# Kernel optimization log

Hardware: AMD Instinct MI355X
Metric: run time of the kernel (lower is better)

## Reference

```python
import jax, jax.numpy as jnp
import numpy as np

B, T, C, H = 2, 2048, 1024, 16
HS = C // H        # head dim = 64
HALF = HS // 2     # rope half = 32


def _rope_cos_sin():
    # standard RoPE frequencies over the half-dim
    inv_freq = 1.0 / (10000.0 ** (np.arange(HALF, dtype=np.float32) / HALF))
    t = np.arange(T, dtype=np.float32)
    ang = np.outer(t, inv_freq)  # [T, HALF]
    cos = np.cos(ang)[None, None]  # [1,1,T,HALF]
    sin = np.sin(ang)[None, None]
    return jnp.asarray(cos), jnp.asarray(sin)


def setup_inputs() -> dict:
    key = jax.random.key(0)
    k1, k2, k3 = jax.random.split(key, 3)
    cos, sin = _rope_cos_sin()
    return {
        "x": jax.random.normal(k1, (B, T, C), dtype=jnp.float32),
        "cos": cos,
        "sin": sin,
        "w_attn": jax.random.normal(k2, (C, 3 * C), dtype=jnp.float32) * (1.0 / np.sqrt(C)),
        "b_attn": jnp.zeros((3 * C,), dtype=jnp.float32),
        "w_proj": jax.random.normal(k3, (C, C), dtype=jnp.float32) * (1.0 / np.sqrt(C)),
        "b_proj": jnp.zeros((C,), dtype=jnp.float32),
    }


def _rope_apply(x, cos, sin):
    # x: [B,H,T,HS]; cos/sin: [1,1,T,HALF]
    x1, x2 = x[..., :HALF], x[..., HALF:]
    return jnp.concatenate([x1 * cos - x2 * sin, x1 * sin + x2 * cos], axis=-1)


def reference(x, cos, sin, w_attn, b_attn, w_proj, b_proj):
    b, t, c = x.shape
    qkv = x @ w_attn + b_attn                      # [B,T,3C]
    q, k, v = jnp.split(qkv, 3, axis=-1)
    # [B,T,C] -> [B,H,T,HS]
    def to_heads(u):
        return u.reshape(b, t, H, HS).transpose(0, 2, 1, 3)
    q, k, v = to_heads(q), to_heads(k), to_heads(v)
    q = _rope_apply(q, cos[:, :, :t], sin[:, :, :t])
    k = _rope_apply(k, cos[:, :, :t], sin[:, :, :t])
    scale = 1.0 / np.sqrt(HS).astype(np.float32)
    scores = jnp.einsum("bhqd,bhkd->bhqk", q, k) * scale
    causal = jnp.tril(jnp.ones((t, t), dtype=bool))
    scores = jnp.where(causal, scores, jnp.finfo(scores.dtype).min)
    attn = jax.nn.softmax(scores, axis=-1)
    ctx = jnp.einsum("bhqk,bhkd->bhqd", attn, v)   # [B,H,T,HS]
    ctx = ctx.transpose(0, 2, 1, 3).reshape(b, t, c)
    return ctx @ w_proj + b_proj
```

## Files before the change

kernel.cpp:

```cpp
#include <hip/hip_runtime.h>
#include <hip/hip_bf16.h>

#define Bn    2
#define Tdim  2048
#define Cdim  1024
#define Hn    16
#define HSd   64
#define Mrows 4096

typedef unsigned short u16;
typedef __attribute__((ext_vector_type(8))) short short8;
typedef __attribute__((ext_vector_type(4))) float f32x4;

__device__ __forceinline__ u16 f2bf(float f) {
  union { __hip_bfloat16 h; u16 u; } cv;
  cv.h = __float2bfloat16(f);
  return cv.u;
}

#define GLOAD_LDS16(g, l)                                                     \
  __builtin_amdgcn_global_load_lds(                                           \
      (const __attribute__((address_space(1))) void*)(g),                     \
      (__attribute__((address_space(3))) void*)(l), 16, 0, 0)

__global__ __launch_bounds__(256) void k_convert_x(const float* __restrict__ x,
                                                   u16* __restrict__ xb) {
  int i = blockIdx.x * 256 + threadIdx.x;
  float4 v = ((const float4*)x)[i];
  unsigned o0 = (unsigned)f2bf(v.x) | ((unsigned)f2bf(v.y) << 16);
  unsigned o1 = (unsigned)f2bf(v.z) | ((unsigned)f2bf(v.w) << 16);
  ((uint2*)xb)[i] = make_uint2(o0, o1);
}

__global__ __launch_bounds__(256) void k_transpose_w(const float* __restrict__ in,
                                                     u16* __restrict__ out,
                                                     int R, int Cc) {
  __shared__ float tile[64][65];
  int c0 = blockIdx.x * 64, r0 = blockIdx.y * 64;
  int lc = threadIdx.x & 63, l0 = threadIdx.x >> 6;
  for (int rr = l0; rr < 64; rr += 4)
    tile[rr][lc] = in[(size_t)(r0 + rr) * Cc + c0 + lc];
  __syncthreads();
  for (int rr = l0; rr < 64; rr += 4)
    out[(size_t)(c0 + rr) * R + r0 + lc] = f2bf(tile[lc][rr]);
}

__global__ __launch_bounds__(256) void k_transpose_v(const u16* __restrict__ Vh,
                                                     u16* __restrict__ Vt) {
  __shared__ u16 tile[64][72];
  int bh = blockIdx.y, t0 = blockIdx.x * 64;
  int lc = threadIdx.x & 63, l0 = threadIdx.x >> 6;
  const u16* src = Vh + (size_t)bh * Tdim * HSd;
  u16* dst = Vt + (size_t)bh * HSd * Tdim;
  for (int rr = l0; rr < 64; rr += 4)
    tile[rr][lc] = src[(size_t)(t0 + rr) * HSd + lc];
  __syncthreads();
  for (int dd = l0; dd < 64; dd += 4)
    dst[(size_t)dd * Tdim + t0 + lc] = tile[lc][dd];
}

template <int EPI>
__global__ __launch_bounds__(256, 2) void k_gemm(
    const u16* __restrict__ A, const u16* __restrict__ Bt,
    const float* __restrict__ bias, const float* __restrict__ cosT,
    const float* __restrict__ sinT, u16* __restrict__ Qh, u16* __restrict__ Kh,
    u16* __restrict__ Vh, float* __restrict__ Out, int Ndim, int Kdim) {
  __shared__ u16 As[128 * 32];
  __shared__ u16 Bs[128 * 32];
  const int tid = threadIdx.x;
  const int wid = tid >> 6, lane = tid & 63;
  const int m0 = blockIdx.x * 128, n0 = blockIdx.y * 128;
  const int wm = (wid >> 1) * 64, wn = (wid & 1) * 64;
  const int lr = lane & 15, lg = lane >> 4;

  f32x4 acc[4][4] = {};

  const u16* Ag = A + (size_t)m0 * Kdim;
  const u16* Bg = Bt + (size_t)n0 * Kdim;
  const int srow = lane >> 2, ske = (lane & 3) * 8;

  for (int k0 = 0; k0 < Kdim; k0 += 32) {
    for (int c = wid; c < 8; c += 4) {
      int row = c * 16 + srow;
      GLOAD_LDS16(Ag + (size_t)row * Kdim + k0 + ske, As + c * 512);
      GLOAD_LDS16(Bg + (size_t)row * Kdim + k0 + ske, Bs + c * 512);
    }
    __syncthreads();
    short8 a[4], b[4];
#pragma unroll
    for (int i = 0; i < 4; i++)
      a[i] = *(const short8*)(As + (wm + i * 16 + lr) * 32 + 8 * lg);
#pragma unroll
    for (int j = 0; j < 4; j++)
      b[j] = *(const short8*)(Bs + (wn + j * 16 + lr) * 32 + 8 * lg);
#pragma unroll
    for (int i = 0; i < 4; i++)
#pragma unroll
      for (int j = 0; j < 4; j++)
        acc[i][j] =
            __builtin_amdgcn_mfma_f32_16x16x32_bf16(a[i], b[j], acc[i][j], 0, 0, 0);
    __syncthreads();
  }

  const int nbase = n0 + wn;
  if (EPI == 0) {
    const int sec = nbase >> 10;
    const int hh = (nbase & 1023) >> 6;
    const float qs = (sec == 0) ? 0.125f : 1.0f;
    float bj[4];
#pragma unroll
    for (int j = 0; j < 4; j++) bj[j] = bias[nbase + j * 16 + lr];
#pragma unroll
    for (int i = 0; i < 4; i++) {
      int growb = m0 + wm + i * 16 + 4 * lg;
#pragma unroll
      for (int r = 0; r < 4; r++) {
        int gr = growb + r;
        int bI = gr >> 11, t = gr & (Tdim - 1);
        size_t off = ((size_t)(bI * Hn + hh) * Tdim + t) * HSd;
        if (sec < 2) {
          u16* dst = (sec == 0) ? Qh : Kh;
#pragma unroll
          for (int j = 0; j < 2; j++) {
            int d = j * 16 + lr;
            float v1 = acc[i][j][r] + bj[j];
            float v2 = acc[i][j + 2][r] + bj[j + 2];
            float cs = cosT[t * 32 + d], sn = sinT[t * 32 + d];
            dst[off + d] = f2bf((v1 * cs - v2 * sn) * qs);
            dst[off + d + 32] = f2bf((v1 * sn + v2 * cs) * qs);
          }
        } else {
#pragma unroll
          for (int j = 0; j < 4; j++)
            Vh[off + j * 16 + lr] = f2bf(acc[i][j][r] + bj[j]);
        }
      }
    }
  } else {
#pragma unroll
    for (int i = 0; i < 4; i++) {
      int growb = m0 + wm + i * 16 + 4 * lg;
#pragma unroll
      for (int r = 0; r < 4; r++) {
        int gr = growb + r;
#pragma unroll
        for (int j = 0; j < 4; j++) {
          int col = nbase + j * 16 + lr;
          Out[(size_t)gr * Ndim + col] = acc[i][j][r] + bias[col];
        }
      }
    }
  }
}

__global__ __launch_bounds__(512, 4) void k_attn(const u16* __restrict__ Qh,
                                                 const u16* __restrict__ Kh,
                                                 const u16* __restrict__ Vt,
                                                 u16* __restrict__ ctx) {
  __shared__ u16 Ks[2][64 * 64];
  __shared__ u16 Vs[2][64 * 64];
  __shared__ u16 Plds[8][16][72];
  const int tid = threadIdx.x;
  const int wid = tid >> 6, lane = tid & 63;
  const int lr = lane & 15, lg = lane >> 4;
  const int bid = blockIdx.x;
  const int xb = 15 - (bid >> 5);
  const int bh = bid & 31;
  const int qr0 = xb * 128 + wid * 16;
  const int nt = 2 * xb + 2;
  const int itd = qr0 >> 6;
  const u16* Q = Qh + (size_t)bh * Tdim * HSd;
  const u16* K = Kh + (size_t)bh * Tdim * HSd;
  const u16* V = Vt + (size_t)bh * HSd * Tdim;

  short8 qf0 = *(const short8*)(Q + (size_t)(qr0 + lr) * HSd + 8 * lg);
  short8 qf1 = *(const short8*)(Q + (size_t)(qr0 + lr) * HSd + 32 + 8 * lg);

  const int srow = lane >> 3;
  const int scol = 16 * ((lane & 7) ^ srow);
  const int swz = (lr & 7) << 4;

  f32x4 ctxa[4] = {};
  float m2[4] = {-1e30f, -1e30f, -1e30f, -1e30f};
  float m2L[4] = {-1e30f, -1e30f, -1e30f, -1e30f};
  float ssum[4] = {0.f, 0.f, 0.f, 0.f};
  const float L2E = 1.44269504089f;
  const f32x4 zero = {};

#define STAGE_KV(b, kv0)                                                      \
  do {                                                                        \
    GLOAD_LDS16((const char*)(K + (size_t)((kv0) + wid * 8 + srow) * HSd) +   \
                    scol,                                                     \
                Ks[b] + wid * 8 * 64);                                        \
    GLOAD_LDS16((const char*)(V + (size_t)(wid * 8 + srow) * Tdim + (kv0)) +  \
                    scol,                                                     \
                Vs[b] + wid * 8 * 64);                                        \
  } while (0)

  STAGE_KV(0, 0);
  __syncthreads();

  int cur = 0;
  for (int it = 0; it < nt; ++it) {
    const int kv0 = it * 64;
    if (it + 1 < nt) STAGE_KV(cur ^ 1, kv0 + 64);

    if (it <= itd) {
      const char* ksb = (const char*)(Ks[cur]);
      const char* vsb = (const char*)(Vs[cur]);

      f32x4 s[4];
#pragma unroll
      for (int f = 0; f < 4; ++f) {
        int row = 16 * f + lr;
        int c0 = (lg * 16) ^ swz;
        short8 kf0 = *(const short8*)(ksb + row * 128 + c0);
        short8 kf1 = *(const short8*)(ksb + row * 128 + (c0 ^ 64));
        s[f] = __builtin_amdgcn_mfma_f32_16x16x32_bf16(qf0, kf0, zero, 0, 0, 0);
        s[f] = __builtin_amdgcn_mfma_f32_16x16x32_bf16(qf1, kf1, s[f], 0, 0, 0);
      }

      float sv[4][4], tm[4];
#pragma unroll
      for (int r = 0; r < 4; ++r) {
        if (it == itd) {
          int q = qr0 + 4 * lg + r;
#pragma unroll
          for (int f = 0; f < 4; ++f)
            sv[f][r] = (kv0 + 16 * f + lr <= q) ? s[f][r] : -1e30f;
        } else {
#pragma unroll
          for (int f = 0; f < 4; ++f) sv[f][r] = s[f][r];
        }
        float t = fmaxf(fmaxf(sv[0][r], sv[1][r]), fmaxf(sv[2][r], sv[3][r]));
        t = fmaxf(t, __shfl_xor(t, 1));
        t = fmaxf(t, __shfl_xor(t, 2));
        t = fmaxf(t, __shfl_xor(t, 4));
        t = fmaxf(t, __shfl_xor(t, 8));
        tm[r] = t;
      }

      bool up = (tm[0] > m2[0]) | (tm[1] > m2[1]) | (tm[2] > m2[2]) |
                (tm[3] > m2[3]);
      if (__any(up)) {
#pragma unroll
        for (int r = 0; r < 4; ++r) {
          float mn = fmaxf(m2[r], tm[r]);
          float alpha = __builtin_amdgcn_exp2f((m2[r] - mn) * L2E);
          m2[r] = mn;
          m2L[r] = mn * L2E;
          ssum[r] *= alpha;
#pragma unroll
          for (int dt = 0; dt < 4; ++dt) ctxa[dt][r] *= alpha;
        }
      }

#pragma unroll
      for (int r = 0; r < 4; ++r) {
#pragma unroll
        for (int f = 0; f < 4; ++f) {
          float p = __builtin_amdgcn_exp2f(fmaf(sv[f][r], L2E, -m2L[r]));
          ssum[r] += p;
          Plds[wid][4 * lg + r][16 * f + lr] = f2bf(p);
        }
      }

      const char* pb = (const char*)(&Plds[wid][0][0]);
      short8 pa0 = *(const short8*)(pb + lr * 144 + lg * 16);
      short8 pa1 = *(const short8*)(pb + lr * 144 + 64 + lg * 16);

#pragma unroll
      for (int dt = 0; dt < 4; ++dt) {
        int row = 16 * dt + lr;
        int c0 = (lg * 16) ^ swz;
        short8 vb0 = *(const short8*)(vsb + row * 128 + c0);
        short8 vb1 = *(const short8*)(vsb + row * 128 + (c0 ^ 64));
        ctxa[dt] =
            __builtin_amdgcn_mfma_f32_16x16x32_bf16(pa0, vb0, ctxa[dt], 0, 0, 0);
        ctxa[dt] =
            __builtin_amdgcn_mfma_f32_16x16x32_bf16(pa1, vb1, ctxa[dt], 0, 0, 0);
      }
    }

    __syncthreads();
    cur ^= 1;
  }
#undef STAGE_KV

  const int bI = bh >> 4, hh = bh & 15;
#pragma unroll
  for (int r = 0; r < 4; ++r) {
    float s = ssum[r];
    s += __shfl_xor(s, 1);
    s += __shfl_xor(s, 2);
    s += __shfl_xor(s, 4);
    s += __shfl_xor(s, 8);
    float inv = 1.0f / s;
    int t = qr0 + 4 * lg + r;
    size_t off = ((size_t)bI * Tdim + t) * Cdim + hh * HSd;
#pragma unroll
    for (int dt = 0; dt < 4; dt++)
      ctx[off + dt * 16 + lr] = f2bf(ctxa[dt][r] * inv);
  }
}

extern "C" void kernel_launch(void* const* d_in, const int* in_sizes, int n_in,
                              void* d_out, int out_size, void* d_ws,
                              size_t ws_size, hipStream_t stream) {
  const float* x = (const float*)d_in[0];
  const float* cosT = (const float*)d_in[1];
  const float* sinT = (const float*)d_in[2];
  const float* wattn = (const float*)d_in[3];
  const float* battn = (const float*)d_in[4];
  const float* wproj = (const float*)d_in[5];
  const float* bproj = (const float*)d_in[6];
  float* out = (float*)d_out;
  char* ws = (char*)d_ws;
  const size_t MB = 1024 * 1024;
  u16* xb = (u16*)(ws + 0);
  u16* Vt = (u16*)(ws + 0);
  u16* wattnT = (u16*)(ws + 8 * MB);
  u16* wprojT = (u16*)(ws + 14 * MB);
  u16* Qh = (u16*)(ws + 16 * MB);
  u16* Kh = (u16*)(ws + 24 * MB);
  u16* Vh = (u16*)(ws + 32 * MB);
  u16* ctx = (u16*)(ws + 40 * MB);

  k_convert_x<<<4096, 256, 0, stream>>>(x, xb);
  k_transpose_w<<<dim3(48, 16), 256, 0, stream>>>(wattn, wattnT, 1024, 3072);
  k_transpose_w<<<dim3(16, 16), 256, 0, stream>>>(wproj, wprojT, 1024, 1024);
  k_gemm<0><<<dim3(32, 24), 256, 0, stream>>>(xb, wattnT, battn, cosT, sinT, Qh,
                                              Kh, Vh, nullptr, 3072, 1024);
  k_transpose_v<<<dim3(32, 32), 256, 0, stream>>>(Vh, Vt);
  k_attn<<<512, 512, 0, stream>>>(Qh, Kh, Vt, ctx);
  k_gemm<1><<<dim3(32, 8), 256, 0, stream>>>(ctx, wprojT, bproj, nullptr,
                                             nullptr, nullptr, nullptr, nullptr,
                                             out, 1024, 1024);
}
```

Baseline: 225.5 us.

## Double-buffer GEMM LDS tiles with K=64 steps and XOR swizzle

The bf16 GEMM kernel now stages 64-wide K tiles into two LDS buffers and prefetches the next tile with direct global-to-LDS loads while computing on the current one. This removes one of the two barriers per iteration and halves the loop trip count. An XOR swizzle on the 16-byte column chunks is meant to cut LDS bank conflicts on the fragment reads. LDS use grows from 16KB to 64KB per block, which can limit how many blocks fit per CU under the launch bound of two.

```diff
diff --git a/kernel.cpp b/kernel.cpp
--- a/kernel.cpp
+++ b/kernel.cpp
@@ -65,42 +65,69 @@
     const float* __restrict__ bias, const float* __restrict__ cosT,
     const float* __restrict__ sinT, u16* __restrict__ Qh, u16* __restrict__ Kh,
     u16* __restrict__ Vh, float* __restrict__ Out, int Ndim, int Kdim) {
-  __shared__ u16 As[128 * 32];
-  __shared__ u16 Bs[128 * 32];
+  __shared__ u16 As[2][128 * 64];
+  __shared__ u16 Bs[2][128 * 64];
   const int tid = threadIdx.x;
   const int wid = tid >> 6, lane = tid & 63;
   const int m0 = blockIdx.x * 128, n0 = blockIdx.y * 128;
   const int wm = (wid >> 1) * 64, wn = (wid & 1) * 64;
   const int lr = lane & 15, lg = lane >> 4;
+  const int swz = (lr & 7) << 4;
 
   f32x4 acc[4][4] = {};
 
   const u16* Ag = A + (size_t)m0 * Kdim;
   const u16* Bg = Bt + (size_t)n0 * Kdim;
-  const int srow = lane >> 2, ske = (lane & 3) * 8;
-
-  for (int k0 = 0; k0 < Kdim; k0 += 32) {
-    for (int c = wid; c < 8; c += 4) {
-      int row = c * 16 + srow;
-      GLOAD_LDS16(Ag + (size_t)row * Kdim + k0 + ske, As + c * 512);
-      GLOAD_LDS16(Bg + (size_t)row * Kdim + k0 + ske, Bs + c * 512);
-    }
+  const int sr8 = lane >> 3;
+  const int scol = 16 * ((lane & 7) ^ sr8);
+
+#define STAGE_G(b, k0)                                                        \
+  do {                                                                        \
+    _Pragma("unroll") for (int c = 0; c < 4; ++c) {                           \
+      int row = c * 32 + wid * 8 + sr8;                                       \
+      GLOAD_LDS16((const char*)(Ag + (size_t)row * Kdim + (k0)) + scol,       \
+                  (u16*)As[b] + (c * 32 + wid * 8) * 64);                     \
+      GLOAD_LDS16((const char*)(Bg + (size_t)row * Kdim + (k0)) + scol,       \
+                  (u16*)Bs[b] + (c * 32 + wid * 8) * 64);                     \
+    }                                                                         \
+  } while (0)
+
+  const int nt = Kdim >> 6;
+  STAGE_G(0, 0);
+  __syncthreads();
+  int cur = 0;
+  for (int t = 0; t < nt; ++t) {
+    if (t + 1 < nt) STAGE_G(cur ^ 1, (t + 1) * 64);
+    const char* ab = (const char*)As[cur];
+    const char* bb = (const char*)Bs[cur];
+    short8 a[4][2], b[4][2];
+#pragma unroll
+    for (int i = 0; i < 4; i++) {
+      int ra = (wm + i * 16 + lr) * 128;
+#pragma unroll
+      for (int kk = 0; kk < 2; kk++)
+        a[i][kk] = *(const short8*)(ab + ra + ((kk * 64 + lg * 16) ^ swz));
+    }
+#pragma unroll
+    for (int j = 0; j < 4; j++) {
+      int rb = (wn + j * 16 + lr) * 128;
+#pragma unroll
+      for (int kk = 0; kk < 2; kk++)
+        b[j][kk] = *(const short8*)(bb + rb + ((kk * 64 + lg * 16) ^ swz));
+    }
+#pragma unroll
+    for (int i = 0; i < 4; i++)
+#pragma unroll
+      for (int j = 0; j < 4; j++) {
+        acc[i][j] = __builtin_amdgcn_mfma_f32_16x16x32_bf16(a[i][0], b[j][0],
+                                                            acc[i][j], 0, 0, 0);
+        acc[i][j] = __builtin_amdgcn_mfma_f32_16x16x32_bf16(a[i][1], b[j][1],
+                                                            acc[i][j], 0, 0, 0);
+      }
     __syncthreads();
-    short8 a[4], b[4];
-#pragma unroll
-    for (int i = 0; i < 4; i++)
-      a[i] = *(const short8*)(As + (wm + i * 16 + lr) * 32 + 8 * lg);
-#pragma unroll
-    for (int j = 0; j < 4; j++)
-      b[j] = *(const short8*)(Bs + (wn + j * 16 + lr) * 32 + 8 * lg);
-#pragma unroll
-    for (int i = 0; i < 4; i++)
-#pragma unroll
-      for (int j = 0; j < 4; j++)
-        acc[i][j] =
-            __builtin_amdgcn_mfma_f32_16x16x32_bf16(a[i], b[j], acc[i][j], 0, 0, 0);
-    __syncthreads();
+    cur ^= 1;
   }
+#undef STAGE_G
 
   const int nbase = n0 + wn;
   if (EPI == 0) {
```

New measurement: 229.9 us. Within noise of the previous version (+2.0%).

## Rewrite GEMM with 256x256 tiles, 4-stage async LDS pipeline and swizzle

Applied to the files above, without the earlier changes.

Replaces the 128x128 single-buffered GEMM with a 512-thread 256x256 tile kernel that prefetches three K-steps ahead into a 4-deep LDS ring using direct global-to-LDS loads. It adds an XOR swizzle against LDS bank conflicts and splits each K-step into two MFMA phases with explicit barriers, waitcnts and priority hints. The aim is to hide global load latency and raise data reuse per block. In exchange, both launches use far fewer blocks (192 and 64), which may underfill the GPU.

```diff
diff --git a/kernel.cpp b/kernel.cpp
--- a/kernel.cpp
+++ b/kernel.cpp
@@ -22,6 +22,8 @@
   __builtin_amdgcn_global_load_lds(                                           \
       (const __attribute__((address_space(1))) void*)(g),                     \
       (__attribute__((address_space(3))) void*)(l), 16, 0, 0)
+
+#define CFENCE asm volatile("" ::: "memory")
 
 __global__ __launch_bounds__(256) void k_convert_x(const float* __restrict__ x,
                                                    u16* __restrict__ xb) {
@@ -60,93 +62,157 @@
 }
 
 template <int EPI>
-__global__ __launch_bounds__(256, 2) void k_gemm(
+__global__ __launch_bounds__(512, 2) void k_gemm(
     const u16* __restrict__ A, const u16* __restrict__ Bt,
     const float* __restrict__ bias, const float* __restrict__ cosT,
     const float* __restrict__ sinT, u16* __restrict__ Qh, u16* __restrict__ Kh,
     u16* __restrict__ Vh, float* __restrict__ Out, int Ndim, int Kdim) {
-  __shared__ u16 As[128 * 32];
-  __shared__ u16 Bs[128 * 32];
+  __shared__ u16 As[4][8192];
+  __shared__ u16 Bs[4][8192];
   const int tid = threadIdx.x;
   const int wid = tid >> 6, lane = tid & 63;
-  const int m0 = blockIdx.x * 128, n0 = blockIdx.y * 128;
-  const int wm = (wid >> 1) * 64, wn = (wid & 1) * 64;
+  const int wr = wid >> 2, wc = wid & 3;
   const int lr = lane & 15, lg = lane >> 4;
-
-  f32x4 acc[4][4] = {};
+  const int m0 = blockIdx.x * 256, n0 = blockIdx.y * 256;
+
+  f32x4 acc[8][4] = {};
 
   const u16* Ag = A + (size_t)m0 * Kdim;
   const u16* Bg = Bt + (size_t)n0 * Kdim;
-  const int srow = lane >> 2, ske = (lane & 3) * 8;
-
-  for (int k0 = 0; k0 < Kdim; k0 += 32) {
-    for (int c = wid; c < 8; c += 4) {
-      int row = c * 16 + srow;
-      GLOAD_LDS16(Ag + (size_t)row * Kdim + k0 + ske, As + c * 512);
-      GLOAD_LDS16(Bg + (size_t)row * Kdim + k0 + ske, Bs + c * 512);
+  const int sgr = wid * 16 + (lane >> 2);
+  const int scb = ((lane & 3) ^ ((lane >> 3) & 3)) << 4;
+
+#define STAGE_A(b, t, i)                                                      \
+  GLOAD_LDS16((const char*)(Ag + (size_t)((i)*128 + sgr) * Kdim + (t)*32) +   \
+                  scb,                                                        \
+              As[b] + (i)*4096 + wid * 512)
+#define STAGE_B(b, t, i)                                                      \
+  GLOAD_LDS16((const char*)(Bg + (size_t)((i)*128 + sgr) * Kdim + (t)*32) +   \
+                  scb,                                                        \
+              Bs[b] + (i)*4096 + wid * 512)
+
+#define LDFRAG(buf, row)                                                      \
+  (*(const short8*)((const char*)(buf) + (row)*64 +                           \
+                    ((lg * 16) ^ ((((row) >> 1) & 3) << 4))))
+
+  const int nt = Kdim >> 5;
+#pragma unroll
+  for (int t = 0; t < 3; ++t) {
+    STAGE_A(t, t, 0);
+    STAGE_A(t, t, 1);
+    STAGE_B(t, t, 0);
+    STAGE_B(t, t, 1);
+  }
+  asm volatile("s_waitcnt vmcnt(8)" ::: "memory");
+  __builtin_amdgcn_s_barrier();
+  CFENCE;
+
+  for (int t = 0; t < nt; ++t) {
+    const u16* ab = As[t & 3];
+    const u16* bb = Bs[t & 3];
+    const int bst = (t + 3) & 3;
+    const bool do_stage = (t + 3 < nt);
+    short8 a[4], b[4];
+#pragma unroll
+    for (int mi = 0; mi < 4; ++mi) a[mi] = LDFRAG(ab, wr * 128 + mi * 16 + lr);
+#pragma unroll
+    for (int nj = 0; nj < 4; ++nj) b[nj] = LDFRAG(bb, wc * 64 + nj * 16 + lr);
+    if (do_stage) {
+      STAGE_A(bst, t + 3, 0);
+      STAGE_A(bst, t + 3, 1);
     }
-    __syncthreads();
-    short8 a[4], b[4];
-#pragma unroll
-    for (int i = 0; i < 4; i++)
-      a[i] = *(const short8*)(As + (wm + i * 16 + lr) * 32 + 8 * lg);
-#pragma unroll
-    for (int j = 0; j < 4; j++)
-      b[j] = *(const short8*)(Bs + (wn + j * 16 + lr) * 32 + 8 * lg);
-#pragma unroll
-    for (int i = 0; i < 4; i++)
-#pragma unroll
-      for (int j = 0; j < 4; j++)
-        acc[i][j] =
-            __builtin_amdgcn_mfma_f32_16x16x32_bf16(a[i], b[j], acc[i][j], 0, 0, 0);
-    __syncthreads();
+    CFENCE;
+    __builtin_amdgcn_s_barrier();
+    asm volatile("s_waitcnt lgkmcnt(0)" ::: "memory");
+    __builtin_amdgcn_sched_barrier(0);
+    __builtin_amdgcn_s_setprio(1);
+#pragma unroll
+    for (int mi = 0; mi < 4; ++mi)
+#pragma unroll
+      for (int nj = 0; nj < 4; ++nj)
+        acc[mi][nj] =
+            __builtin_amdgcn_mfma_f32_16x16x32_bf16(a[mi], b[nj], acc[mi][nj], 0, 0, 0);
+    __builtin_amdgcn_s_setprio(0);
+    CFENCE;
+    __builtin_amdgcn_s_barrier();
+    CFENCE;
+#pragma unroll
+    for (int mi = 0; mi < 4; ++mi)
+      a[mi] = LDFRAG(ab, wr * 128 + (mi + 4) * 16 + lr);
+    if (do_stage) {
+      STAGE_B(bst, t + 3, 0);
+      STAGE_B(bst, t + 3, 1);
+    }
+    if (t + 4 <= nt)
+      asm volatile("s_waitcnt vmcnt(8)" ::: "memory");
+    else if (t + 3 == nt)
+      asm volatile("s_waitcnt vmcnt(4)" ::: "memory");
+    else if (t + 2 == nt)
+      asm volatile("s_waitcnt vmcnt(0)" ::: "memory");
+    __builtin_amdgcn_s_barrier();
+    asm volatile("s_waitcnt lgkmcnt(0)" ::: "memory");
+    __builtin_amdgcn_sched_barrier(0);
+    __builtin_amdgcn_s_setprio(1);
+#pragma unroll
+    for (int mi = 0; mi < 4; ++mi)
+#pragma unroll
+      for (int nj = 0; nj < 4; ++nj)
+        acc[mi + 4][nj] = __builtin_amdgcn_mfma_f32_16x16x32_bf16(
+            a[mi], b[nj], acc[mi + 4][nj], 0, 0, 0);
+    __builtin_amdgcn_s_setprio(0);
+    CFENCE;
+    __builtin_amdgcn_s_barrier();
+    CFENCE;
   }
-
-  const int nbase = n0 + wn;
+#undef STAGE_A
+#undef STAGE_B
+#undef LDFRAG
+
+  const int nbase = n0 + wc * 64;
   if (EPI == 0) {
     const int sec = nbase >> 10;
     const int hh = (nbase & 1023) >> 6;
     const float qs = (sec == 0) ? 0.125f : 1.0f;
     float bj[4];
 #pragma unroll
-    for (int j = 0; j < 4; j++) bj[j] = bias[nbase + j * 16 + lr];
-#pragma unroll
-    for (int i = 0; i < 4; i++) {
-      int growb = m0 + wm + i * 16 + 4 * lg;
-#pragma unroll
-      for (int r = 0; r < 4; r++) {
+    for (int nj = 0; nj < 4; ++nj) bj[nj] = bias[nbase + nj * 16 + lr];
+#pragma unroll
+    for (int mi = 0; mi < 8; ++mi) {
+      int growb = m0 + wr * 128 + mi * 16 + 4 * lg;
+#pragma unroll
+      for (int r = 0; r < 4; ++r) {
         int gr = growb + r;
-        int bI = gr >> 11, t = gr & (Tdim - 1);
-        size_t off = ((size_t)(bI * Hn + hh) * Tdim + t) * HSd;
+        int bI = gr >> 11, tq = gr & (Tdim - 1);
+        size_t off = ((size_t)(bI * Hn + hh) * Tdim + tq) * HSd;
         if (sec < 2) {
           u16* dst = (sec == 0) ? Qh : Kh;
 #pragma unroll
-          for (int j = 0; j < 2; j++) {
-            int d = j * 16 + lr;
-            float v1 = acc[i][j][r] + bj[j];
-            float v2 = acc[i][j + 2][r] + bj[j + 2];
-            float cs = cosT[t * 32 + d], sn = sinT[t * 32 + d];
+          for (int nj = 0; nj < 2; ++nj) {
+            int d = nj * 16 + lr;
+            float v1 = acc[mi][nj][r] + bj[nj];
+            float v2 = acc[mi][nj + 2][r] + bj[nj + 2];
+            float cs = cosT[tq * 32 + d], sn = sinT[tq * 32 + d];
             dst[off + d] = f2bf((v1 * cs - v2 * sn) * qs);
             dst[off + d + 32] = f2bf((v1 * sn + v2 * cs) * qs);
           }
         } else {
 #pragma unroll
-          for (int j = 0; j < 4; j++)
-            Vh[off + j * 16 + lr] = f2bf(acc[i][j][r] + bj[j]);
+          for (int nj = 0; nj < 4; ++nj)
+            Vh[off + nj * 16 + lr] = f2bf(acc[mi][nj][r] + bj[nj]);
         }
       }
     }
   } else {
 #pragma unroll
-    for (int i = 0; i < 4; i++) {
-      int growb = m0 + wm + i * 16 + 4 * lg;
-#pragma unroll
-      for (int r = 0; r < 4; r++) {
+    for (int mi = 0; mi < 8; ++mi) {
+      int growb = m0 + wr * 128 + mi * 16 + 4 * lg;
+#pragma unroll
+      for (int r = 0; r < 4; ++r) {
         int gr = growb + r;
 #pragma unroll
-        for (int j = 0; j < 4; j++) {
-          int col = nbase + j * 16 + lr;
-          Out[(size_t)gr * Ndim + col] = acc[i][j][r] + bias[col];
+        for (int nj = 0; nj < 4; ++nj) {
+          int col = nbase + nj * 16 + lr;
+          Out[(size_t)gr * Ndim + col] = acc[mi][nj][r] + bias[col];
         }
       }
     }
@@ -329,11 +395,11 @@
   k_convert_x<<<4096, 256, 0, stream>>>(x, xb);
   k_transpose_w<<<dim3(48, 16), 256, 0, stream>>>(wattn, wattnT, 1024, 3072);
   k_transpose_w<<<dim3(16, 16), 256, 0, stream>>>(wproj, wprojT, 1024, 1024);
-  k_gemm<0><<<dim3(32, 24), 256, 0, stream>>>(xb, wattnT, battn, cosT, sinT, Qh,
-                                              Kh, Vh, nullptr, 3072, 1024);
+  k_gemm<0><<<dim3(16, 12), 512, 0, stream>>>(xb, wattnT, battn, cosT, sinT,
+                                              Qh, Kh, Vh, nullptr, 3072, 1024);
   k_transpose_v<<<dim3(32, 32), 256, 0, stream>>>(Vh, Vt);
   k_attn<<<512, 512, 0, stream>>>(Qh, Kh, Vt, ctx);
-  k_gemm<1><<<dim3(32, 8), 256, 0, stream>>>(ctx, wprojT, bproj, nullptr,
+  k_gemm<1><<<dim3(16, 4), 512, 0, stream>>>(ctx, wprojT, bproj, nullptr,
                                              nullptr, nullptr, nullptr, nullptr,
                                              out, 1024, 1024);
 }
```

New measurement: 242.3 us. 1.07x slower.
